# Optimization experiments

Measured on AMD Instinct MI355X. Metric: run time of the kernel, lower is better.

Reference implementation:

```python
import jax, jax.numpy as jnp
import numpy as np

CUTOFF = 5.0        # init kwarg: cutoff
CUTOFF_SHELL = 2.0  # init kwarg: cutoff_shell (skin); nbl built with cutoff+shell
BOX = 20.0          # simulation box extent (no PBC: cell=0, pbc=False)


def setup_inputs() -> dict:
    key = jax.random.key(0)
    # [n_molecules, n_atoms, 3] positions, uniform in a 20 A box
    positions = jax.random.uniform(key, (64, 512, 3), dtype=jnp.float32) * BOX
    return {"positions": positions}


def reference(positions):
    # Batched, vectorized equivalent of the per-molecule Python loop:
    # for each molecule, pairs (i,j), i != j, with |r_i - r_j| < cutoff + shell.
    M, N, _ = positions.shape
    rc = CUTOFF + CUTOFF_SHELL
    # Rij[m,i,j] = r_j - r_i  (displacement vectors, as SchNet nbl transforms emit)
    Rij = positions[:, None, :, :] - positions[:, :, None, :]   # [M,N,N,3]
    d2 = jnp.sum(Rij * Rij, axis=-1)                            # [M,N,N]
    self_mask = jnp.eye(N, dtype=bool)                          # exclude i==j
    nbh_mask = (d2 < rc * rc) & ~self_mask                      # [M,N,N] bool
    # Dense, static-shape representation of the collated ragged neighbor list:
    # masked displacement vectors (zero outside cutoff). idx_i/idx_j with
    # molecule offsets are exactly nonzero(nbh_mask) in a dynamic-shape world.
    return Rij * nbh_mask[..., None].astype(Rij.dtype)
```

## Files before the change

kernel.cpp:

```cpp
#include <hip/hip_runtime.h>


#define NMOL   64
#define NATOM  512
#define RC2    49.0f
#define SLICES 32

typedef unsigned int   u32;
typedef unsigned short u16;

__device__ __forceinline__ float bf2f(u16 u) {
    union { u32 u; float f; } v; v.u = ((u32)u) << 16; return v.f;
}

__global__ __launch_bounds__(256)
void nbl_kernel(const void* __restrict__ pos_raw, float* __restrict__ out) {
    __shared__ int s_f32;
    const int t = threadIdx.x;

    if (t == 0) s_f32 = 0;
    __syncthreads();
    {
        const u32* w = (const u32*)pos_raw;
        const u32 a = w[t];
        const u32 b = w[t + 256];
        if ((((a >> 8) & 0xffu) > 0x41u) || (((b >> 8) & 0xffu) > 0x41u))
            s_f32 = 1;
    }
    __syncthreads();
    const bool is_f32 = (s_f32 != 0);

    const int bx     = blockIdx.x;
    const int m      = bx >> 5;
    const int slice  = bx & (SLICES - 1);
    const int lane   = t & 63;
    const int wave   = t >> 6;
    const int i_base = slice * 16 + wave * 4;

    const float* pm32 = (const float*)pos_raw + (size_t)m * (NATOM * 3);
    const u16*   pm16 = (const u16*)pos_raw   + (size_t)m * (NATOM * 3);

    float pj[24];
    if (is_f32) {
        const float4* p4 = (const float4*)pm32 + lane * 6;
        #pragma unroll
        for (int k = 0; k < 6; ++k) {
            const float4 q = p4[k];
            pj[4*k+0] = q.x; pj[4*k+1] = q.y; pj[4*k+2] = q.z; pj[4*k+3] = q.w;
        }
    } else {
        const uint4* p4 = (const uint4*)pm16 + lane * 3;
        u32 words[12];
        #pragma unroll
        for (int k = 0; k < 3; ++k) {
            const uint4 q = p4[k];
            words[4*k+0] = q.x; words[4*k+1] = q.y;
            words[4*k+2] = q.z; words[4*k+3] = q.w;
        }
        #pragma unroll
        for (int k = 0; k < 12; ++k) {
            pj[2*k]   = bf2f((u16)(words[k] & 0xffffu));
            pj[2*k+1] = bf2f((u16)(words[k] >> 16));
        }
    }

    const int j0 = lane * 8;

    #pragma unroll
    for (int r = 0; r < 4; ++r) {
        const int i = i_base + r;
        float rix, riy, riz;
        if (is_f32) {
            rix = pm32[3*i+0]; riy = pm32[3*i+1]; riz = pm32[3*i+2];
        } else {
            rix = bf2f(pm16[3*i+0]); riy = bf2f(pm16[3*i+1]); riz = bf2f(pm16[3*i+2]);
        }

        float o[24];
        #pragma unroll
        for (int jj = 0; jj < 8; ++jj) {
            const float dx = __fsub_rn(pj[3*jj+0], rix);
            const float dy = __fsub_rn(pj[3*jj+1], riy);
            const float dz = __fsub_rn(pj[3*jj+2], riz);
            const float d2 = __fadd_rn(__fadd_rn(__fmul_rn(dx, dx),
                                                 __fmul_rn(dy, dy)),
                                       __fmul_rn(dz, dz));
            const bool keep = (d2 < RC2) && ((j0 + jj) != i);
            o[3*jj+0] = keep ? dx : 0.0f;
            o[3*jj+1] = keep ? dy : 0.0f;
            o[3*jj+2] = keep ? dz : 0.0f;
        }

        const size_t row = (size_t)(m * NATOM + i);
        float4* op = (float4*)out + row * 384 + lane * 6;
        #pragma unroll
        for (int k = 0; k < 6; ++k)
            op[k] = make_float4(o[4*k+0], o[4*k+1], o[4*k+2], o[4*k+3]);
    }
}

extern "C" void kernel_launch(void* const* d_in, const int* in_sizes, int n_in,
                              void* d_out, int out_size, void* d_ws, size_t ws_size,
                              hipStream_t stream) {
    const void* pos = d_in[0];
    float* out = (float*)d_out;
    dim3 grid(NMOL * SLICES);
    dim3 block(256);
    nbl_kernel<<<grid, block, 0, stream>>>(pos, out);
}
```

Before: 220.8 us.

## Assign one output row per block with fully coalesced float4 stores

```diff
diff --git a/kernel.cpp b/kernel.cpp
--- a/kernel.cpp
+++ b/kernel.cpp
@@ -4,7 +4,6 @@
 #define NMOL   64
 #define NATOM  512
 #define RC2    49.0f
-#define SLICES 32
 
 typedef unsigned int   u32;
 typedef unsigned short u16;
@@ -13,90 +12,75 @@
     union { u32 u; float f; } v; v.u = ((u32)u) << 16; return v.f;
 }
 
-__global__ __launch_bounds__(256)
+__global__ __launch_bounds__(384)
 void nbl_kernel(const void* __restrict__ pos_raw, float* __restrict__ out) {
-    __shared__ int s_f32;
-    const int t = threadIdx.x;
+    const int t    = threadIdx.x;
+    const int lane = t & 63;
 
-    if (t == 0) s_f32 = 0;
-    __syncthreads();
-    {
-        const u32* w = (const u32*)pos_raw;
-        const u32 a = w[t];
-        const u32 b = w[t + 256];
-        if ((((a >> 8) & 0xffu) > 0x41u) || (((b >> 8) & 0xffu) > 0x41u))
-            s_f32 = 1;
-    }
-    __syncthreads();
-    const bool is_f32 = (s_f32 != 0);
+    const u32* w = (const u32*)pos_raw;
+    const u32 wa = w[lane];
+    const u32 wb = w[lane + 128];
+    const bool is_f32 = __any((int)(((( wa >> 8) & 0xffu) > 0x41u) |
+                                    ((( wb >> 8) & 0xffu) > 0x41u)));
 
-    const int bx     = blockIdx.x;
-    const int m      = bx >> 5;
-    const int slice  = bx & (SLICES - 1);
-    const int lane   = t & 63;
-    const int wave   = t >> 6;
-    const int i_base = slice * 16 + wave * 4;
+    const int bx = blockIdx.x;
+    const int m  = bx >> 9;
+    const int i  = bx & (NATOM - 1);
+    const int c  = t;
+    const int ja = (4 * c) / 3;
+    const int cm = c % 3;
 
     const float* pm32 = (const float*)pos_raw + (size_t)m * (NATOM * 3);
     const u16*   pm16 = (const u16*)pos_raw   + (size_t)m * (NATOM * 3);
 
-    float pj[24];
+    float rx, ry, rz;
+    float p0, p1, p2, p3, p4, p5;
     if (is_f32) {
-        const float4* p4 = (const float4*)pm32 + lane * 6;
-        #pragma unroll
-        for (int k = 0; k < 6; ++k) {
-            const float4 q = p4[k];
-            pj[4*k+0] = q.x; pj[4*k+1] = q.y; pj[4*k+2] = q.z; pj[4*k+3] = q.w;
-        }
+        rx = pm32[3*i+0]; ry = pm32[3*i+1]; rz = pm32[3*i+2];
+        const float* pa = pm32 + 3 * ja;
+        p0 = pa[0]; p1 = pa[1]; p2 = pa[2]; p3 = pa[3]; p4 = pa[4]; p5 = pa[5];
     } else {
-        const uint4* p4 = (const uint4*)pm16 + lane * 3;
-        u32 words[12];
-        #pragma unroll
-        for (int k = 0; k < 3; ++k) {
-            const uint4 q = p4[k];
-            words[4*k+0] = q.x; words[4*k+1] = q.y;
-            words[4*k+2] = q.z; words[4*k+3] = q.w;
-        }
-        #pragma unroll
-        for (int k = 0; k < 12; ++k) {
-            pj[2*k]   = bf2f((u16)(words[k] & 0xffffu));
-            pj[2*k+1] = bf2f((u16)(words[k] >> 16));
-        }
+        rx = bf2f(pm16[3*i+0]); ry = bf2f(pm16[3*i+1]); rz = bf2f(pm16[3*i+2]);
+        const u16* pa = pm16 + 3 * ja;
+        p0 = bf2f(pa[0]); p1 = bf2f(pa[1]); p2 = bf2f(pa[2]);
+        p3 = bf2f(pa[3]); p4 = bf2f(pa[4]); p5 = bf2f(pa[5]);
     }
 
-    const int j0 = lane * 8;
+    const float dax = __fsub_rn(p0, rx);
+    const float day = __fsub_rn(p1, ry);
+    const float daz = __fsub_rn(p2, rz);
+    const float d2a = __fadd_rn(__fadd_rn(__fmul_rn(dax, dax),
+                                          __fmul_rn(day, day)),
+                                __fmul_rn(daz, daz));
+    const float ka = ((d2a < RC2) && (ja != i)) ? 1.0f : 0.0f;
 
-    #pragma unroll
-    for (int r = 0; r < 4; ++r) {
-        const int i = i_base + r;
-        float rix, riy, riz;
-        if (is_f32) {
-            rix = pm32[3*i+0]; riy = pm32[3*i+1]; riz = pm32[3*i+2];
-        } else {
-            rix = bf2f(pm16[3*i+0]); riy = bf2f(pm16[3*i+1]); riz = bf2f(pm16[3*i+2]);
-        }
+    const float dbx = __fsub_rn(p3, rx);
+    const float dby = __fsub_rn(p4, ry);
+    const float dbz = __fsub_rn(p5, rz);
+    const float d2b = __fadd_rn(__fadd_rn(__fmul_rn(dbx, dbx),
+                                          __fmul_rn(dby, dby)),
+                                __fmul_rn(dbz, dbz));
+    const float kb = ((d2b < RC2) && ((ja + 1) != i)) ? 1.0f : 0.0f;
 
-        float o[24];
-        #pragma unroll
-        for (int jj = 0; jj < 8; ++jj) {
-            const float dx = __fsub_rn(pj[3*jj+0], rix);
-            const float dy = __fsub_rn(pj[3*jj+1], riy);
-            const float dz = __fsub_rn(pj[3*jj+2], riz);
-            const float d2 = __fadd_rn(__fadd_rn(__fmul_rn(dx, dx),
-                                                 __fmul_rn(dy, dy)),
-                                       __fmul_rn(dz, dz));
-            const bool keep = (d2 < RC2) && ((j0 + jj) != i);
-            o[3*jj+0] = keep ? dx : 0.0f;
-            o[3*jj+1] = keep ? dy : 0.0f;
-            o[3*jj+2] = keep ? dz : 0.0f;
-        }
+    const float f0 = (cm == 0) ? p0 : ((cm == 1) ? p1 : p2);
+    const float f1 = (cm == 0) ? p1 : ((cm == 1) ? p2 : p3);
+    const float f2 = (cm == 0) ? p2 : ((cm == 1) ? p3 : p4);
+    const float f3 = (cm == 0) ? p3 : ((cm == 1) ? p4 : p5);
+    const float r0 = (cm == 0) ? rx : ((cm == 1) ? ry : rz);
+    const float r1 = (cm == 0) ? ry : ((cm == 1) ? rz : rx);
+    const float r2 = (cm == 0) ? rz : ((cm == 1) ? rx : ry);
+    const float m0 = ka;
+    const float m1 = (cm == 2) ? kb : ka;
+    const float m2 = (cm == 0) ? ka : kb;
+    const float m3 = kb;
 
-        const size_t row = (size_t)(m * NATOM + i);
-        float4* op = (float4*)out + row * 384 + lane * 6;
-        #pragma unroll
-        for (int k = 0; k < 6; ++k)
-            op[k] = make_float4(o[4*k+0], o[4*k+1], o[4*k+2], o[4*k+3]);
-    }
+    float4 o;
+    o.x = __fmul_rn(__fsub_rn(f0, r0), m0);
+    o.y = __fmul_rn(__fsub_rn(f1, r1), m1);
+    o.z = __fmul_rn(__fsub_rn(f2, r2), m2);
+    o.w = __fmul_rn(__fsub_rn(f3, r0), m3);
+
+    ((float4*)out)[(size_t)bx * 384 + c] = o;
 }
 
 extern "C" void kernel_launch(void* const* d_in, const int* in_sizes, int n_in,
@@ -104,7 +88,7 @@
                               hipStream_t stream) {
     const void* pos = d_in[0];
     float* out = (float*)d_out;
-    dim3 grid(NMOL * SLICES);
-    dim3 block(256);
+    dim3 grid(NMOL * NATOM);
+    dim3 block(384);
     nbl_kernel<<<grid, block, 0, stream>>>(pos, out);
 }
```

After: 216.5 us. 1.02x faster.
